# Optimization experiments

Hardware: AMD Instinct MI355X
Metric: run time of the kernel (lower is better)

The kernel has to match this reference:

```python
import jax, jax.numpy as jnp
import numpy as np

D_HIDDEN = 1024
NUM_HEADS = 16
D_HEAD = D_HIDDEN // NUM_HEADS


def setup_inputs() -> dict:
    key = jax.random.key(0)
    ks = jax.random.split(key, 9)
    N, S, D = 4, 2048, D_HIDDEN
    s = 1.0 / np.sqrt(D)
    inp = {
        "x": jax.random.normal(ks[0], (N, S, D), dtype=jnp.float32),
        "Wq": jax.random.uniform(ks[1], (D, D), jnp.float32, -s, s),
        "bq": jnp.zeros((D,), jnp.float32),
        "Wk": jax.random.uniform(ks[2], (D, D), jnp.float32, -s, s),
        "bk": jnp.zeros((D,), jnp.float32),
        "Wv": jax.random.uniform(ks[3], (D, D), jnp.float32, -s, s),
        "bv": jnp.zeros((D,), jnp.float32),
        "Wo": jax.random.uniform(ks[4], (D, D), jnp.float32, -s, s),
        "bo": jnp.zeros((D,), jnp.float32),
        "ln_gamma": jnp.ones((D,), jnp.float32),
        "ln_beta": jnp.zeros((D,), jnp.float32),
    }
    return inp


def _layer_norm(x, gamma, beta, eps=1e-5):
    mu = jnp.mean(x, axis=-1, keepdims=True)
    var = jnp.var(x, axis=-1, keepdims=True)
    return (x - mu) * jax.lax.rsqrt(var + eps) * gamma + beta


def reference(x, Wq, bq, Wk, bk, Wv, bv, Wo, bo, ln_gamma, ln_beta):
    N, S, D = x.shape
    H, Dh = NUM_HEADS, D_HEAD
    xn = _layer_norm(x, ln_gamma, ln_beta)
    # torch Linear: y = x @ W.T + b
    q = (xn @ Wq.T + bq).reshape(N, S, H, Dh)
    k = (xn @ Wk.T + bk).reshape(N, S, H, Dh)
    v = (xn @ Wv.T + bv).reshape(N, S, H, Dh)
    # scores: [N, H, S, S]
    scores = jnp.einsum('nxhd,nyhd->nhxy', q, k) / np.sqrt(Dh)
    # causal mask: positions y > x get -inf
    mask = jnp.triu(jnp.full((S, S), -jnp.inf, dtype=scores.dtype), k=1)
    attn = jax.nn.softmax(scores + mask[None, None], axis=-1)
    z = jnp.einsum('nhxy,nyhd->nxhd', attn, v).reshape(N, S, D)
    return z @ Wo.T + bo
```

## Files before the change

### kernel.cpp

```cpp
#include <hip/hip_runtime.h>

typedef unsigned short u16;
typedef unsigned int   u32;
typedef __bf16 bf16x8 __attribute__((ext_vector_type(8)));
typedef float  f32x4  __attribute__((ext_vector_type(4)));
typedef unsigned short u16x8 __attribute__((ext_vector_type(8)));
typedef unsigned short u16x4 __attribute__((ext_vector_type(4)));

#define SEQ 2048
#define DM  1024
#define TOKS 8388608
#define SCLQ 0.18033688f

__device__ __forceinline__ float bf2f(u16 u) {
    u32 i = ((u32)u) << 16;
    float f; __builtin_memcpy(&f, &i, 4); return f;
}
__device__ __forceinline__ u16 f2bf(float f) {
    u32 i; __builtin_memcpy(&i, &f, 4);
    return (u16)((i + 0x7FFFu + ((i >> 16) & 1u)) >> 16);
}
__device__ __forceinline__ bf16x8 ld8(const u16* p) {
    return __builtin_bit_cast(bf16x8, *(const u16x8*)p);
}
#define GLD16(src, dst) __builtin_amdgcn_global_load_lds( \
    (const __attribute__((address_space(1))) void*)(src), \
    (__attribute__((address_space(3))) void*)(dst), 16, 0, 0)

__global__ __launch_bounds__(64) void detect_k(const u32* __restrict__ x, int* __restrict__ flag) {
    const int lane = threadIdx.x;
    u32 w = x[lane];
    int e0 = (int)((w >> 7) & 0xFFu);
    int cnt = (e0 >= 100 && e0 <= 140) ? 1 : 0;
#pragma unroll
    for (int off = 32; off; off >>= 1) cnt += __shfl_xor(cnt, off);
    if (lane == 0) *flag = (cnt < 32) ? 1 : 0;
}

__global__ __launch_bounds__(256) void convert_k(const void* s0, const void* s1, const void* s2, const void* s3,
                                                 const void* v0, const void* v1, const void* v2, const void* v3,
                                                 const void* v4, const void* v5,
                                                 u16* __restrict__ dstW, u16* __restrict__ dstV,
                                                 const int* __restrict__ flagp) {
    const int y = blockIdx.y, tid = threadIdx.x;
    const int fp32m = *flagp;
    const void* src; u16* dst; size_t off;
    if (y < 4) {
        src = (y == 0) ? s0 : (y == 1) ? s1 : (y == 2) ? s2 : s3;
        dst = dstW + (size_t)y * 1048576;
        off = (size_t)blockIdx.x * 1024 + tid * 4;
    } else {
        const int i = blockIdx.x;
        if (i >= 6) return;
        src = (i == 0) ? v0 : (i == 1) ? v1 : (i == 2) ? v2 : (i == 3) ? v3 : (i == 4) ? v4 : v5;
        dst = dstV + (size_t)i * 1024;
        off = (size_t)tid * 4;
    }
    u16x4 o;
    if (fp32m) {
        const float* f = (const float*)src + off;
#pragma unroll
        for (int j = 0; j < 4; ++j) o[j] = f2bf(f[j]);
    } else {
        o = *(const u16x4*)((const u16*)src + off);
    }
    *(u16x4*)(dst + off) = o;
}

__global__ __launch_bounds__(256) void ln_k(const void* __restrict__ xv,
                                            const u16* __restrict__ g,
                                            const u16* __restrict__ b,
                                            u16* __restrict__ xn,
                                            const int* __restrict__ flagp) {
    const int row = blockIdx.x, tid = threadIdx.x;
    const int fp32m = *flagp;
    float f[4], s1 = 0.f, s2 = 0.f;
    if (fp32m) {
        f32x4 v = *(const f32x4*)((const float*)xv + (size_t)row * DM + tid * 4);
#pragma unroll
        for (int j = 0; j < 4; ++j) f[j] = v[j];
    } else {
        u16x4 v = *(const u16x4*)((const u16*)xv + (size_t)row * DM + tid * 4);
#pragma unroll
        for (int j = 0; j < 4; ++j) f[j] = bf2f(v[j]);
    }
#pragma unroll
    for (int j = 0; j < 4; ++j) { s1 += f[j]; s2 += f[j] * f[j]; }
#pragma unroll
    for (int off = 32; off; off >>= 1) { s1 += __shfl_xor(s1, off); s2 += __shfl_xor(s2, off); }
    __shared__ float red[8];
    const int wave = tid >> 6, lane = tid & 63;
    if (lane == 0) { red[wave] = s1; red[4 + wave] = s2; }
    __syncthreads();
    s1 = red[0] + red[1] + red[2] + red[3];
    s2 = red[4] + red[5] + red[6] + red[7];
    const float mu = s1 * (1.f / DM);
    const float var = s2 * (1.f / DM) - mu * mu;
    const float rs = rsqrtf(var + 1e-5f);
    u16x4 gv = *(const u16x4*)(g + tid * 4);
    u16x4 bv = *(const u16x4*)(b + tid * 4);
    u16x4 o;
#pragma unroll
    for (int j = 0; j < 4; ++j) o[j] = f2bf((f[j] - mu) * rs * bf2f(gv[j]) + bf2f(bv[j]));
    *(u16x4*)(xn + (size_t)row * DM + tid * 4) = o;
}

template <int VT>
__device__ __forceinline__ void gemm_core(u16* As, u16* Bs,
                                          const u16* __restrict__ A,
                                          const u16* __restrict__ W,
                                          const u16* __restrict__ bias,
                                          u16* __restrict__ out,
                                          const int* __restrict__ flagp,
                                          float scale) {
    const int tid = threadIdx.x, wave = tid >> 6, lane = tid & 63;
    const int l4 = lane & 15, q4 = lane >> 4;
    const int bm = blockIdx.x, bn = blockIdx.y;
    const int wm = (wave >> 1) * 64, wn = (wave & 1) * 64;
    int fp32m = 0;
    if (VT == 2) fp32m = *flagp;
    f32x4 acc[4][4] = {};
    const int srow = wave * 32 + (lane >> 2);
    const int skoff = (lane & 3) * 8;
    const u16* Ag = A + ((size_t)(bm * 128 + srow)) * DM + skoff;
    const u16* Wg = W + ((size_t)(bn * 128 + srow)) * DM + skoff;
    u16* As0 = As + wave * 1024;
    u16* Bs0 = Bs + wave * 1024;

    for (int k0 = 0; k0 < DM; k0 += 32) {
        GLD16(Ag + k0, As0);
        GLD16(Ag + 16 * DM + k0, As0 + 512);
        GLD16(Wg + k0, Bs0);
        GLD16(Wg + 16 * DM + k0, Bs0 + 512);
        __syncthreads();
        bf16x8 af[4], bfr[4];
#pragma unroll
        for (int t = 0; t < 4; ++t)
            af[t] = ld8(As + (wm + t * 16 + l4) * 32 + q4 * 8);
#pragma unroll
        for (int t = 0; t < 4; ++t)
            bfr[t] = ld8(Bs + (wn + t * 16 + l4) * 32 + q4 * 8);
#pragma unroll
        for (int mt = 0; mt < 4; ++mt)
#pragma unroll
            for (int nt = 0; nt < 4; ++nt)
                acc[mt][nt] = __builtin_amdgcn_mfma_f32_16x16x32_bf16(af[mt], bfr[nt], acc[mt][nt], 0, 0, 0);
        __syncthreads();
    }

#pragma unroll
    for (int nt = 0; nt < 4; ++nt) {
        const int col = bn * 128 + wn + nt * 16 + l4;
        const float bs = bf2f(bias[col]);
#pragma unroll
        for (int mt = 0; mt < 4; ++mt) {
            const int row0 = bm * 128 + wm + mt * 16 + q4 * 4;
            if (VT == 1) {
                const int nb = row0 >> 11, s0 = row0 & 2047;
                u16x4 pk;
#pragma unroll
                for (int r = 0; r < 4; ++r) pk[r] = f2bf((acc[mt][nt][r] + bs) * scale);
                *(u16x4*)(out + ((size_t)(nb * 1024 + col)) * SEQ + s0) = pk;
            } else if (VT == 2 && fp32m) {
#pragma unroll
                for (int r = 0; r < 4; ++r)
                    ((float*)out)[(size_t)(row0 + r) * DM + col] = acc[mt][nt][r] + bs;
            } else {
#pragma unroll
                for (int r = 0; r < 4; ++r)
                    out[(size_t)(row0 + r) * DM + col] = f2bf((acc[mt][nt][r] + bs) * scale);
            }
        }
    }
}

__global__ __launch_bounds__(256) void gemm_qkv_k(const u16* __restrict__ xn, const u16* __restrict__ Wc,
                                                  const u16* __restrict__ Vc,
                                                  u16* __restrict__ Q, u16* __restrict__ K, u16* __restrict__ Vt) {
    __shared__ alignas(16) u16 As[128 * 32];
    __shared__ alignas(16) u16 Bs[128 * 32];
    const int z = blockIdx.z;
    if (z == 0)      gemm_core<0>(As, Bs, xn, Wc,               Vc,        Q,  nullptr, SCLQ);
    else if (z == 1) gemm_core<0>(As, Bs, xn, Wc + 1048576,     Vc + 1024, K,  nullptr, 1.0f);
    else             gemm_core<1>(As, Bs, xn, Wc + 2 * 1048576, Vc + 2048, Vt, nullptr, 1.0f);
}

__global__ __launch_bounds__(256) void gemm_out_k(const u16* __restrict__ Z, const u16* __restrict__ Wc,
                                                  const u16* __restrict__ Vc,
                                                  u16* __restrict__ out, const int* __restrict__ flagp) {
    __shared__ alignas(16) u16 As[128 * 32];
    __shared__ alignas(16) u16 Bs[128 * 32];
    gemm_core<2>(As, Bs, Z, Wc + 3 * 1048576, Vc + 3 * 1024, out, flagp, 1.0f);
}

__global__ __launch_bounds__(256, 4) void flash_k(const u16* __restrict__ Q,
                                                  const u16* __restrict__ K,
                                                  const u16* __restrict__ Vt,
                                                  u16* __restrict__ Z) {
    const int bh = blockIdx.x;
    const int qb = 15 - (int)blockIdx.y;
    const int n = bh >> 4, h = bh & 15;
    const int tid = threadIdx.x, wave = tid >> 6, lane = tid & 63;
    const int l4 = lane & 15, q4 = lane >> 4;

    __shared__ alignas(16) u16 Ks[2][64 * 32];
    __shared__ alignas(16) u16 Vs[2][64 * 32];
    __shared__ alignas(16) u16 Pl[4][2][16 * 72];

    const int Q0w = qb * 128 + wave * 32;
    bf16x8 qf[2][2];
#pragma unroll
    for (int qt = 0; qt < 2; ++qt) {
        const u16* Qr = Q + ((size_t)(n * SEQ + Q0w + qt * 16 + l4)) * DM + h * 64 + q4 * 8;
        qf[qt][0] = ld8(Qr);
        qf[qt][1] = ld8(Qr + 32);
    }

    const int srow = lane >> 2, scol = (lane & 3) * 8;
    const u16* Kg = K + ((size_t)(n * SEQ + wave * 16 + srow)) * DM + h * 64 + scol;
    const u16* Vg = Vt + ((size_t)(n * 1024 + h * 64 + wave * 16 + srow)) * SEQ + scol;
    u16* KsD0 = &Ks[0][wave * 512];
    u16* KsD1 = &Ks[1][wave * 512];
    u16* VsD0 = &Vs[0][wave * 512];
    u16* VsD1 = &Vs[1][wave * 512];

    f32x4 o[2][4] = {};
    float l_acc[2] = {0.f, 0.f};
    const int nch = 2 * qb + 2;

    for (int c = 0; c < nch; ++c) {
        const int kv0 = c * 64;
        const size_t krow = (size_t)kv0 * DM;
        GLD16(Kg + krow, KsD0);
        GLD16(Kg + krow + 32, KsD1);
        GLD16(Vg + kv0, VsD0);
        GLD16(Vg + kv0 + 32, VsD1);
        __syncthreads();

        bf16x8 a[4][2];
#pragma unroll
        for (int mt = 0; mt < 4; ++mt) {
            a[mt][0] = ld8(&Ks[0][(mt * 16 + l4) * 32 + q4 * 8]);
            a[mt][1] = ld8(&Ks[1][(mt * 16 + l4) * 32 + q4 * 8]);
        }
#pragma unroll
        for (int qt = 0; qt < 2; ++qt) {
            f32x4 st[4];
#pragma unroll
            for (int mt = 0; mt < 4; ++mt) {
                f32x4 zz = {0.f, 0.f, 0.f, 0.f};
                st[mt] = __builtin_amdgcn_mfma_f32_16x16x32_bf16(a[mt][0], qf[qt][0], zz, 0, 0, 0);
                st[mt] = __builtin_amdgcn_mfma_f32_16x16x32_bf16(a[mt][1], qf[qt][1], st[mt], 0, 0, 0);
            }
            const int qg = Q0w + qt * 16 + l4;
            u16* P = Pl[wave][qt];
            float la = l_acc[qt];
#pragma unroll
            for (int mt = 0; mt < 4; ++mt) {
                __bf16 pk[4];
#pragma unroll
                for (int r = 0; r < 4; ++r) {
                    const int kv = kv0 + mt * 16 + q4 * 4 + r;
                    float p = __builtin_amdgcn_exp2f(st[mt][r]);
                    p = (kv > qg) ? 0.f : p;
                    la += p;
                    pk[r] = (__bf16)p;
                }
                *(u16x4*)(P + l4 * 72 + mt * 16 + q4 * 4) = *(u16x4*)pk;
            }
            l_acc[qt] = la;
        }
#pragma unroll
        for (int ks = 0; ks < 2; ++ks) {
            bf16x8 pf0 = ld8(&Pl[wave][0][l4 * 72 + ks * 32 + q4 * 8]);
            bf16x8 pf1 = ld8(&Pl[wave][1][l4 * 72 + ks * 32 + q4 * 8]);
#pragma unroll
            for (int nt = 0; nt < 4; ++nt) {
                bf16x8 vf = ld8(&Vs[ks][(nt * 16 + l4) * 32 + q4 * 8]);
                o[0][nt] = __builtin_amdgcn_mfma_f32_16x16x32_bf16(pf0, vf, o[0][nt], 0, 0, 0);
                o[1][nt] = __builtin_amdgcn_mfma_f32_16x16x32_bf16(pf1, vf, o[1][nt], 0, 0, 0);
            }
        }
        __syncthreads();
    }

#pragma unroll
    for (int qt = 0; qt < 2; ++qt) {
        float l = l_acc[qt];
        l += __shfl_xor(l, 16);
        l += __shfl_xor(l, 32);
        float lr[4];
#pragma unroll
        for (int r = 0; r < 4; ++r) lr[r] = 1.f / __shfl(l, q4 * 4 + r);
#pragma unroll
        for (int nt = 0; nt < 4; ++nt) {
            const int col = h * 64 + nt * 16 + l4;
#pragma unroll
            for (int r = 0; r < 4; ++r) {
                const int row = n * SEQ + Q0w + qt * 16 + q4 * 4 + r;
                Z[(size_t)row * DM + col] = f2bf(o[qt][nt][r] * lr[r]);
            }
        }
    }
}

extern "C" void kernel_launch(void* const* d_in, const int* in_sizes, int n_in,
                              void* d_out, int out_size, void* d_ws, size_t ws_size,
                              hipStream_t stream) {
    const void* x  = d_in[0];
    const void* Wq = d_in[1];
    const void* bq = d_in[2];
    const void* Wk = d_in[3];
    const void* bk = d_in[4];
    const void* Wv = d_in[5];
    const void* bv = d_in[6];
    const void* Wo = d_in[7];
    const void* bo = d_in[8];
    const void* g  = d_in[9];
    const void* b  = d_in[10];
    u16* ws = (u16*)d_ws;

    u16* xn  = ws;
    u16* Qb  = ws + (size_t)TOKS;
    u16* Kb  = ws + (size_t)2 * TOKS;
    u16* Vtb = ws + (size_t)3 * TOKS;
    u16* Zb  = ws;
    u16* Wc  = ws + (size_t)4 * TOKS;
    u16* Vc  = Wc + 4 * 1048576;
    int* flagp = (int*)(Vc + 8 * 1024);

    detect_k<<<dim3(1), 64, 0, stream>>>((const u32*)x, flagp);
    convert_k<<<dim3(1024, 5), 256, 0, stream>>>(Wq, Wk, Wv, Wo, bq, bk, bv, bo, g, b, Wc, Vc, flagp);
    ln_k<<<dim3(4 * SEQ), 256, 0, stream>>>(x, Vc + 4 * 1024, Vc + 5 * 1024, xn, flagp);
    gemm_qkv_k<<<dim3(64, 8, 3), 256, 0, stream>>>(xn, Wc, Vc, Qb, Kb, Vtb);
    flash_k<<<dim3(64, 16), 256, 0, stream>>>(Qb, Kb, Vtb, Zb);
    gemm_out_k<<<dim3(64, 8), 256, 0, stream>>>(Zb, Wc, Vc, (u16*)d_out, flagp);
}
```

Measured before the change: 259.3 us.

## Rewrite projection GEMMs as 256x128 tiles with triple-buffered async LDS pipeline

Result: faster. 250.4 us (-3.4%).

```diff
diff --git a/kernel.cpp b/kernel.cpp
--- a/kernel.cpp
+++ b/kernel.cpp
@@ -105,92 +105,169 @@
     *(u16x4*)(xn + (size_t)row * DM + tid * 4) = o;
 }
 
-template <int VT>
-__device__ __forceinline__ void gemm_core(u16* As, u16* Bs,
-                                          const u16* __restrict__ A,
-                                          const u16* __restrict__ W,
-                                          const u16* __restrict__ bias,
-                                          u16* __restrict__ out,
-                                          const int* __restrict__ flagp,
-                                          float scale) {
-    const int tid = threadIdx.x, wave = tid >> 6, lane = tid & 63;
+
+#define LDS_U16 73728
+
+__device__ __forceinline__ void wait_vm12() { asm volatile("s_waitcnt vmcnt(12)" ::: "memory"); }
+__device__ __forceinline__ void wait_vm6()  { asm volatile("s_waitcnt vmcnt(6)"  ::: "memory"); }
+__device__ __forceinline__ void wait_vm0()  { asm volatile("s_waitcnt vmcnt(0)"  ::: "memory"); }
+
+template <int EPI>
+__device__ __forceinline__ void gemm256x128(u16* lds,
+                                            const u16* __restrict__ A,
+                                            const u16* __restrict__ W,
+                                            const u16* __restrict__ bias,
+                                            u16* __restrict__ o0, u16* __restrict__ o1, u16* __restrict__ o2,
+                                            int fp32m) {
+    const int tid = threadIdx.x;
+    const int w = tid >> 6, lane = tid & 63;
     const int l4 = lane & 15, q4 = lane >> 4;
     const int bm = blockIdx.x, bn = blockIdx.y;
-    const int wm = (wave >> 1) * 64, wn = (wave & 1) * 64;
-    int fp32m = 0;
-    if (VT == 2) fp32m = *flagp;
+    const int wm = (w >> 1) * 64, wn = (w & 1) * 64;
+
+    const int srow = lane >> 3;
+    const int schk = (lane & 7) ^ srow;
+    const u16* sA = A + ((size_t)(bm * 256 + w * 32 + srow)) * DM + (schk << 3);
+    const u16* sB = W + ((size_t)(bn * 128 + w * 16 + srow)) * DM + (schk << 3);
+
+    int offA[4][2], offB[4][2];
+#pragma unroll
+    for (int mt = 0; mt < 4; ++mt)
+#pragma unroll
+        for (int s = 0; s < 2; ++s) {
+            const int row = wm + mt * 16 + l4;
+            offA[mt][s] = row * 64 + (((s * 4 + q4) ^ (l4 & 7)) << 3);
+        }
+#pragma unroll
+    for (int nt = 0; nt < 4; ++nt)
+#pragma unroll
+        for (int s = 0; s < 2; ++s) {
+            const int row = wn + nt * 16 + l4;
+            offB[nt][s] = 16384 + row * 64 + (((s * 4 + q4) ^ (l4 & 7)) << 3);
+        }
+
+    auto STAGE = [&](int kt, int b) {
+        const u16* a0 = sA + kt * 64;
+        const u16* b0 = sB + kt * 64;
+        u16* la = lds + b * 24576 + w * 2048;
+        u16* lb = lds + b * 24576 + 16384 + w * 1024;
+        GLD16(a0,           la);
+        GLD16(a0 + 8 * DM,  la + 512);
+        GLD16(a0 + 16 * DM, la + 1024);
+        GLD16(a0 + 24 * DM, la + 1536);
+        GLD16(b0,           lb);
+        GLD16(b0 + 8 * DM,  lb + 512);
+    };
+
     f32x4 acc[4][4] = {};
-    const int srow = wave * 32 + (lane >> 2);
-    const int skoff = (lane & 3) * 8;
-    const u16* Ag = A + ((size_t)(bm * 128 + srow)) * DM + skoff;
-    const u16* Wg = W + ((size_t)(bn * 128 + srow)) * DM + skoff;
-    u16* As0 = As + wave * 1024;
-    u16* Bs0 = Bs + wave * 1024;
-
-    for (int k0 = 0; k0 < DM; k0 += 32) {
-        GLD16(Ag + k0, As0);
-        GLD16(Ag + 16 * DM + k0, As0 + 512);
-        GLD16(Wg + k0, Bs0);
-        GLD16(Wg + 16 * DM + k0, Bs0 + 512);
-        __syncthreads();
-        bf16x8 af[4], bfr[4];
-#pragma unroll
-        for (int t = 0; t < 4; ++t)
-            af[t] = ld8(As + (wm + t * 16 + l4) * 32 + q4 * 8);
-#pragma unroll
-        for (int t = 0; t < 4; ++t)
-            bfr[t] = ld8(Bs + (wn + t * 16 + l4) * 32 + q4 * 8);
+
+    STAGE(0, 0); STAGE(1, 1); STAGE(2, 2);
+
+#pragma unroll
+    for (int kt = 0; kt < 16; ++kt) {
+        const int b = kt % 3;
+        if (kt < 14)      wait_vm12();
+        else if (kt == 14) wait_vm6();
+        else               wait_vm0();
+        __builtin_amdgcn_s_barrier();
+        __builtin_amdgcn_sched_barrier(0);
+        const u16* base = lds + b * 24576;
+        bf16x8 af[4][2], bfr[4][2];
 #pragma unroll
         for (int mt = 0; mt < 4; ++mt)
 #pragma unroll
-            for (int nt = 0; nt < 4; ++nt)
-                acc[mt][nt] = __builtin_amdgcn_mfma_f32_16x16x32_bf16(af[mt], bfr[nt], acc[mt][nt], 0, 0, 0);
-        __syncthreads();
-    }
-
-#pragma unroll
-    for (int nt = 0; nt < 4; ++nt) {
-        const int col = bn * 128 + wn + nt * 16 + l4;
-        const float bs = bf2f(bias[col]);
-#pragma unroll
-        for (int mt = 0; mt < 4; ++mt) {
-            const int row0 = bm * 128 + wm + mt * 16 + q4 * 4;
-            if (VT == 1) {
-                const int nb = row0 >> 11, s0 = row0 & 2047;
-                u16x4 pk;
-#pragma unroll
-                for (int r = 0; r < 4; ++r) pk[r] = f2bf((acc[mt][nt][r] + bs) * scale);
-                *(u16x4*)(out + ((size_t)(nb * 1024 + col)) * SEQ + s0) = pk;
-            } else if (VT == 2 && fp32m) {
-#pragma unroll
-                for (int r = 0; r < 4; ++r)
-                    ((float*)out)[(size_t)(row0 + r) * DM + col] = acc[mt][nt][r] + bs;
-            } else {
-#pragma unroll
-                for (int r = 0; r < 4; ++r)
-                    out[(size_t)(row0 + r) * DM + col] = f2bf((acc[mt][nt][r] + bs) * scale);
-            }
-        }
-    }
-}
-
-__global__ __launch_bounds__(256) void gemm_qkv_k(const u16* __restrict__ xn, const u16* __restrict__ Wc,
-                                                  const u16* __restrict__ Vc,
-                                                  u16* __restrict__ Q, u16* __restrict__ K, u16* __restrict__ Vt) {
-    __shared__ alignas(16) u16 As[128 * 32];
-    __shared__ alignas(16) u16 Bs[128 * 32];
-    const int z = blockIdx.z;
-    if (z == 0)      gemm_core<0>(As, Bs, xn, Wc,               Vc,        Q,  nullptr, SCLQ);
-    else if (z == 1) gemm_core<0>(As, Bs, xn, Wc + 1048576,     Vc + 1024, K,  nullptr, 1.0f);
-    else             gemm_core<1>(As, Bs, xn, Wc + 2 * 1048576, Vc + 2048, Vt, nullptr, 1.0f);
-}
-
-__global__ __launch_bounds__(256) void gemm_out_k(const u16* __restrict__ Z, const u16* __restrict__ Wc,
-                                                  const u16* __restrict__ Vc,
-                                                  u16* __restrict__ out, const int* __restrict__ flagp) {
-    __shared__ alignas(16) u16 As[128 * 32];
-    __shared__ alignas(16) u16 Bs[128 * 32];
-    gemm_core<2>(As, Bs, Z, Wc + 3 * 1048576, Vc + 3 * 1024, out, flagp, 1.0f);
+            for (int s = 0; s < 2; ++s) af[mt][s] = ld8(base + offA[mt][s]);
+#pragma unroll
+        for (int nt = 0; nt < 2; ++nt)
+#pragma unroll
+            for (int s = 0; s < 2; ++s) bfr[nt][s] = ld8(base + offB[nt][s]);
+        __builtin_amdgcn_s_setprio(1);
+#pragma unroll
+        for (int mt = 0; mt < 4; ++mt)
+#pragma unroll
+            for (int nt = 0; nt < 2; ++nt)
+#pragma unroll
+                for (int s = 0; s < 2; ++s)
+                    acc[mt][nt] = __builtin_amdgcn_mfma_f32_16x16x32_bf16(af[mt][s], bfr[nt][s], acc[mt][nt], 0, 0, 0);
+        __builtin_amdgcn_s_setprio(0);
+#pragma unroll
+        for (int nt = 2; nt < 4; ++nt)
+#pragma unroll
+            for (int s = 0; s < 2; ++s) bfr[nt][s] = ld8(base + offB[nt][s]);
+        __builtin_amdgcn_s_setprio(1);
+#pragma unroll
+        for (int mt = 0; mt < 4; ++mt)
+#pragma unroll
+            for (int nt = 2; nt < 4; ++nt)
+#pragma unroll
+                for (int s = 0; s < 2; ++s)
+                    acc[mt][nt] = __builtin_amdgcn_mfma_f32_16x16x32_bf16(af[mt][s], bfr[nt][s], acc[mt][nt], 0, 0, 0);
+        __builtin_amdgcn_s_setprio(0);
+        __builtin_amdgcn_s_barrier();
+        __builtin_amdgcn_sched_barrier(0);
+        if (kt < 13) STAGE(kt + 3, b);
+    }
+
+    if (EPI == 0) {
+        const int whichB = bn >> 3;
+        const int cb = (bn & 7) * 128 + wn;
+        u16* outp = (whichB == 0) ? o0 : (whichB == 1) ? o1 : o2;
+        const float scl = (whichB == 0) ? SCLQ : 1.0f;
+#pragma unroll
+        for (int nt = 0; nt < 4; ++nt) {
+            const int cc = cb + nt * 16 + l4;
+            const float bs = bf2f(bias[whichB * 1024 + cc]);
+#pragma unroll
+            for (int mt = 0; mt < 4; ++mt) {
+                const int row0 = bm * 256 + wm + mt * 16 + q4 * 4;
+                if (whichB < 2) {
+#pragma unroll
+                    for (int r = 0; r < 4; ++r)
+                        outp[(size_t)(row0 + r) * DM + cc] = f2bf((acc[mt][nt][r] + bs) * scl);
+                } else {
+                    const int nb = row0 >> 11, s0 = row0 & 2047;
+                    u16x4 pk;
+#pragma unroll
+                    for (int r = 0; r < 4; ++r) pk[r] = f2bf(acc[mt][nt][r] + bs);
+                    *(u16x4*)(outp + ((size_t)(nb * 1024 + cc)) * SEQ + s0) = pk;
+                }
+            }
+        }
+    } else {
+#pragma unroll
+        for (int nt = 0; nt < 4; ++nt) {
+            const int cc = bn * 128 + wn + nt * 16 + l4;
+            const float bs = bf2f(bias[cc]);
+#pragma unroll
+            for (int mt = 0; mt < 4; ++mt) {
+                const int row0 = bm * 256 + wm + mt * 16 + q4 * 4;
+                if (fp32m) {
+#pragma unroll
+                    for (int r = 0; r < 4; ++r)
+                        ((float*)o0)[(size_t)(row0 + r) * DM + cc] = acc[mt][nt][r] + bs;
+                } else {
+#pragma unroll
+                    for (int r = 0; r < 4; ++r)
+                        o0[(size_t)(row0 + r) * DM + cc] = f2bf(acc[mt][nt][r] + bs);
+                }
+            }
+        }
+    }
+}
+
+__global__ __launch_bounds__(512, 2) void gemm_qkv_k(const u16* __restrict__ xn, const u16* __restrict__ Wc,
+                                                     const u16* __restrict__ Vc,
+                                                     u16* __restrict__ Q, u16* __restrict__ K, u16* __restrict__ Vt) {
+    __shared__ alignas(16) u16 lds[LDS_U16];
+    gemm256x128<0>(lds, xn, Wc, Vc, Q, K, Vt, 0);
+}
+
+__global__ __launch_bounds__(512, 2) void gemm_out_k(const u16* __restrict__ Z, const u16* __restrict__ Wc,
+                                                     const u16* __restrict__ Vc,
+                                                     u16* __restrict__ out, const int* __restrict__ flagp) {
+    __shared__ alignas(16) u16 lds[LDS_U16];
+    const int fp32m = *flagp;
+    gemm256x128<1>(lds, Z, Wc + 3 * 1048576, Vc + 3 * 1024, out, nullptr, nullptr, fp32m);
 }
 
 __global__ __launch_bounds__(256, 4) void flash_k(const u16* __restrict__ Q,
@@ -332,7 +409,7 @@
     detect_k<<<dim3(1), 64, 0, stream>>>((const u32*)x, flagp);
     convert_k<<<dim3(1024, 5), 256, 0, stream>>>(Wq, Wk, Wv, Wo, bq, bk, bv, bo, g, b, Wc, Vc, flagp);
     ln_k<<<dim3(4 * SEQ), 256, 0, stream>>>(x, Vc + 4 * 1024, Vc + 5 * 1024, xn, flagp);
-    gemm_qkv_k<<<dim3(64, 8, 3), 256, 0, stream>>>(xn, Wc, Vc, Qb, Kb, Vtb);
+    gemm_qkv_k<<<dim3(32, 24), 512, 0, stream>>>(xn, Wc, Vc, Qb, Kb, Vtb);
     flash_k<<<dim3(64, 16), 256, 0, stream>>>(Qb, Kb, Vtb, Zb);
-    gemm_out_k<<<dim3(64, 8), 256, 0, stream>>>(Zb, Wc, Vc, (u16*)d_out, flagp);
-}
+    gemm_out_k<<<dim3(32, 8), 512, 0, stream>>>(Zb, Wc, Vc, (u16*)d_out, flagp);
+}
```
